# Kernel optimization log

Measured on AMD Instinct MI355X. Metric: run time of the kernel, lower is better.

## Reference

```python
import jax, jax.numpy as jnp
import numpy as np
import math

D_MODEL = 512
NUM_HEADS = 8
D_K = D_MODEL // NUM_HEADS
B, S = 8, 2048


def setup_inputs() -> dict:
    key = jax.random.key(0)
    ks = jax.random.split(key, 13)
    inv = 1.0 / math.sqrt(D_MODEL)
    def lin(kw, kb):
        W = jax.random.uniform(kw, (D_MODEL, D_MODEL), jnp.float32, -inv, inv)
        b = jax.random.uniform(kb, (D_MODEL,), jnp.float32, -inv, inv)
        return W, b
    Wq, bq = lin(ks[0], ks[1])
    Wk, bk = lin(ks[2], ks[3])
    Wv, bv = lin(ks[4], ks[5])
    Wo, bo = lin(ks[6], ks[7])
    Q = jax.random.normal(ks[8], (B, S, D_MODEL), jnp.float32)
    K = jax.random.normal(ks[9], (B, S, D_MODEL), jnp.float32)
    V = jax.random.normal(ks[10], (B, S, D_MODEL), jnp.float32)
    mask = jax.random.randint(ks[11], (1, 1, S, S), 0, 2, jnp.int32)
    return {"Q": Q, "K": K, "V": V, "mask": mask,
            "Wq": Wq, "bq": bq, "Wk": Wk, "bk": bk,
            "Wv": Wv, "bv": bv, "Wo": Wo, "bo": bo}


def _split_heads(x):
    b, s, _ = x.shape
    return x.reshape(b, s, NUM_HEADS, D_K).transpose(0, 2, 1, 3)  # [B,H,S,dk]


def reference(Q, K, V, mask, Wq, bq, Wk, bk, Wv, bv, Wo, bo):
    # Linear projections (torch Linear: x @ W^T + b) then head split
    q = _split_heads(Q @ Wq.T + bq)
    k = _split_heads(K @ Wk.T + bk)
    v = _split_heads(V @ Wv.T + bv)
    scores = jnp.einsum("bhqd,bhkd->bhqk", q, k) / math.sqrt(D_K)
    # masked_fill(mask == 0, -1e30) for float32
    scores = jnp.where(mask == 0, jnp.float32(-1e30), scores)
    probs = jax.nn.softmax(scores, axis=-1)
    # dropout in eval mode == identity
    out = jnp.einsum("bhqk,bhkd->bhqd", probs, v)
    out = out.transpose(0, 2, 1, 3).reshape(Q.shape[0], -1, D_MODEL)
    return out @ Wo.T + bo
```

## Files before the change

kernel.cpp:

```cpp
#include <hip/hip_runtime.h>
#include <hip/hip_bf16.h>
#include <math.h>

#define BB 8
#define SS 2048
#define HH 8
#define DKK 64
#define DM 512

typedef short bf16x8 __attribute__((ext_vector_type(8)));
typedef short bf16x4 __attribute__((ext_vector_type(4)));
typedef float f32x4 __attribute__((ext_vector_type(4)));
#define MFMA16(a, b, c) __builtin_amdgcn_mfma_f32_16x16x32_bf16(a, b, c, 0, 0, 0)

#if __has_builtin(__builtin_amdgcn_exp2f)
#define EXP2(x) __builtin_amdgcn_exp2f(x)
#else
#define EXP2(x) exp2f(x)
#endif

__device__ __forceinline__ unsigned short f2bf(float f) {
    __hip_bfloat16 h = __float2bfloat16(f);
    return *reinterpret_cast<unsigned short*>(&h);
}

__device__ __forceinline__ float max3f(float a, float b, float c) {
    return fmaxf(fmaxf(a, b), c);
}

__device__ __forceinline__ uint4 cvt8(const float* __restrict__ src) {
    float4 a = *(const float4*)src;
    float4 b = *(const float4*)(src + 4);
    unsigned short tmp[8];
    tmp[0] = f2bf(a.x); tmp[1] = f2bf(a.y); tmp[2] = f2bf(a.z); tmp[3] = f2bf(a.w);
    tmp[4] = f2bf(b.x); tmp[5] = f2bf(b.y); tmp[6] = f2bf(b.z); tmp[7] = f2bf(b.w);
    return *(uint4*)tmp;
}

__global__ __launch_bounds__(256) void mask_pack(
    const int* __restrict__ mask, unsigned long long* __restrict__ mb)
{
    const int t = threadIdx.x;
    const int wid = (blockIdx.x << 2) | (t >> 6);
    const int lane = t & 63;
    const int q = wid >> 5;
    const int c = wid & 31;
    int e = mask[(size_t)q * SS + (c << 6) + lane];
    unsigned long long bal = __ballot(e != 0);
    if (lane == 0) mb[wid] = bal;
}

__global__ __launch_bounds__(256) void w_cvt(
    const float* __restrict__ Wq, const float* __restrict__ Wk,
    const float* __restrict__ Wv, unsigned short* __restrict__ dst)
{
    const int idx = blockIdx.x * 256 + threadIdx.x;
    const int which = idx >> 15;
    const int off = (idx & 32767) * 8;
    const float* src = (which == 0) ? Wq : (which == 1) ? Wk : Wv;
    *(uint4*)(dst + (size_t)which * 262144 + off) = cvt8(src + off);
}

__global__ __launch_bounds__(256, 2) void proj_qkv_fused(
    const float* __restrict__ Xq, const float* __restrict__ Xk, const float* __restrict__ Xv,
    const unsigned short* __restrict__ Wb,
    const float* __restrict__ bq, const float* __restrict__ bk, const float* __restrict__ bv,
    unsigned short* __restrict__ outbase, float qscale)
{
    const int z = blockIdx.z;
    const float* X = (z == 0) ? Xq : (z == 1) ? Xk : Xv;
    const unsigned short* W = Wb + (size_t)z * 262144;
    const float* bias = (z == 0) ? bq : (z == 1) ? bk : bv;
    unsigned short* out = outbase + (size_t)z * ((size_t)BB * HH * SS * DKK);
    const float scale = (z == 0) ? qscale : 1.0f;

    __shared__ __align__(16) unsigned short Xs[128][72];
    __shared__ __align__(16) unsigned short Ws[128][72];
    const int t = threadIdx.x;
    const int w = t >> 6, l = t & 63;
    const int l15 = l & 15, lg = l >> 4;
    const int n0 = blockIdx.x * 128, m0 = blockIdx.y * 128;
    const int mo = (w & 1) * 64, no = (w >> 1) * 64;

    f32x4 acc[4][4];
#pragma unroll
    for (int i = 0; i < 4; i++)
#pragma unroll
        for (int j = 0; j < 4; j++) acc[i][j] = (f32x4){0.f, 0.f, 0.f, 0.f};

    for (int k0 = 0; k0 < DM; k0 += 64) {
        __syncthreads();
#pragma unroll
        for (int rr = 0; rr < 4; rr++) {
            int idx = rr * 2048 + t * 8;
            int row = idx >> 6, col = idx & 63;
            *(uint4*)&Xs[row][col] = cvt8(X + (size_t)(m0 + row) * DM + k0 + col);
            *(uint4*)&Ws[row][col] = *(const uint4*)(W + (size_t)(n0 + row) * DM + k0 + col);
        }
        __syncthreads();

        bf16x8 af[4][2], bfr[4][2];
#pragma unroll
        for (int mt = 0; mt < 4; mt++) {
            af[mt][0] = *(const bf16x8*)&Xs[mo + mt * 16 + l15][lg * 8];
            af[mt][1] = *(const bf16x8*)&Xs[mo + mt * 16 + l15][32 + lg * 8];
        }
#pragma unroll
        for (int nt = 0; nt < 4; nt++) {
            bfr[nt][0] = *(const bf16x8*)&Ws[no + nt * 16 + l15][lg * 8];
            bfr[nt][1] = *(const bf16x8*)&Ws[no + nt * 16 + l15][32 + lg * 8];
        }
#pragma unroll
        for (int mt = 0; mt < 4; mt++)
#pragma unroll
            for (int nt = 0; nt < 4; nt++) {
                acc[mt][nt] = MFMA16(af[mt][0], bfr[nt][0], acc[mt][nt]);
                acc[mt][nt] = MFMA16(af[mt][1], bfr[nt][1], acc[mt][nt]);
            }
    }

    float bv4[4];
#pragma unroll
    for (int nt = 0; nt < 4; nt++) bv4[nt] = bias[n0 + no + nt * 16 + l15];

    const int h = (n0 + no) >> 6;
    if (z == 2) {
#pragma unroll
        for (int mt = 0; mt < 4; mt++) {
            int m = m0 + mo + mt * 16 + lg * 4;
            int bb = m >> 11, s = m & (SS - 1);
#pragma unroll
            for (int nt = 0; nt < 4; nt++) {
                int d = nt * 16 + l15;
                bf16x4 pk;
#pragma unroll
                for (int r = 0; r < 4; r++) pk[r] = (short)f2bf(acc[mt][nt][r] + bv4[nt]);
                *(bf16x4*)(out + (((size_t)bb * HH + h) * DKK + d) * SS + s) = pk;
            }
        }
    } else {
#pragma unroll
        for (int mt = 0; mt < 4; mt++)
#pragma unroll
            for (int nt = 0; nt < 4; nt++)
#pragma unroll
                for (int r = 0; r < 4; r++) {
                    int m = m0 + mo + mt * 16 + lg * 4 + r;
                    int d = nt * 16 + l15;
                    float v = (acc[mt][nt][r] + bv4[nt]) * scale;
                    int bb = m >> 11, s = m & (SS - 1);
                    out[(((size_t)bb * HH + h) * SS + s) * 64 + d] = f2bf(v);
                }
    }
}

__global__ __launch_bounds__(256, 2) void proj_out_mfma(
    const unsigned short* __restrict__ Xb,
    const float* __restrict__ W,
    const float* __restrict__ bias,
    float* __restrict__ out)
{
    __shared__ __align__(16) unsigned short Xs[128][72];
    __shared__ __align__(16) unsigned short Ws[128][72];
    const int t = threadIdx.x;
    const int w = t >> 6, l = t & 63;
    const int l15 = l & 15, lg = l >> 4;
    const int n0 = blockIdx.x * 128, m0 = blockIdx.y * 128;
    const int mo = (w & 1) * 64, no = (w >> 1) * 64;

    f32x4 acc[4][4];
#pragma unroll
    for (int i = 0; i < 4; i++)
#pragma unroll
        for (int j = 0; j < 4; j++) acc[i][j] = (f32x4){0.f, 0.f, 0.f, 0.f};

    for (int k0 = 0; k0 < DM; k0 += 64) {
        __syncthreads();
#pragma unroll
        for (int rr = 0; rr < 4; rr++) {
            int idx = rr * 2048 + t * 8;
            int row = idx >> 6, col = idx & 63;
            *(uint4*)&Xs[row][col] = *(const uint4*)(Xb + (size_t)(m0 + row) * DM + k0 + col);
            *(uint4*)&Ws[row][col] = cvt8(W + (size_t)(n0 + row) * DM + k0 + col);
        }
        __syncthreads();

        bf16x8 af[4][2], bfr[4][2];
#pragma unroll
        for (int mt = 0; mt < 4; mt++) {
            af[mt][0] = *(const bf16x8*)&Xs[mo + mt * 16 + l15][lg * 8];
            af[mt][1] = *(const bf16x8*)&Xs[mo + mt * 16 + l15][32 + lg * 8];
        }
#pragma unroll
        for (int nt = 0; nt < 4; nt++) {
            bfr[nt][0] = *(const bf16x8*)&Ws[no + nt * 16 + l15][lg * 8];
            bfr[nt][1] = *(const bf16x8*)&Ws[no + nt * 16 + l15][32 + lg * 8];
        }
#pragma unroll
        for (int mt = 0; mt < 4; mt++)
#pragma unroll
            for (int nt = 0; nt < 4; nt++) {
                acc[mt][nt] = MFMA16(af[mt][0], bfr[nt][0], acc[mt][nt]);
                acc[mt][nt] = MFMA16(af[mt][1], bfr[nt][1], acc[mt][nt]);
            }
    }

    float bv4[4];
#pragma unroll
    for (int nt = 0; nt < 4; nt++) bv4[nt] = bias[n0 + no + nt * 16 + l15];

#pragma unroll
    for (int mt = 0; mt < 4; mt++)
#pragma unroll
        for (int nt = 0; nt < 4; nt++)
#pragma unroll
            for (int r = 0; r < 4; r++) {
                int m = m0 + mo + mt * 16 + lg * 4 + r;
                int n = n0 + no + nt * 16 + l15;
                out[(size_t)m * DM + n] = acc[mt][nt][r] + bv4[nt];
            }
}

__global__ __launch_bounds__(512, 4) void attn_kernel(
    const unsigned short* __restrict__ qw, const unsigned short* __restrict__ kw,
    const unsigned short* __restrict__ vtw,
    const unsigned long long* __restrict__ mb,
    unsigned short* __restrict__ ao)
{
    __shared__ __align__(16) unsigned short Ks[64][72];
    __shared__ __align__(16) unsigned short Vt[64][72];
    __shared__ __align__(16) unsigned short Pw[8 * 32 * 64];
    const int t = threadIdx.x;
    const int w = t >> 6, l = t & 63;
    const int l15 = l & 15, lg = l >> 4;
    const int q0 = blockIdx.x * 256;
    const int bh = blockIdx.y;
    const int b = bh >> 3, h = bh & 7;
    const int q0w = q0 + w * 32;
    const unsigned short* qb = qw + (size_t)bh * SS * DKK;
    const unsigned short* kb = kw + (size_t)bh * SS * DKK;
    const unsigned short* vtb = vtw + (size_t)bh * DKK * SS;

    const unsigned long long* mbq[2];
#pragma unroll
    for (int qt = 0; qt < 2; qt++)
        mbq[qt] = mb + ((size_t)(q0w + qt * 16 + l15) << 5);

    bf16x8 Qf[2][2];
#pragma unroll
    for (int qt = 0; qt < 2; qt++)
#pragma unroll
        for (int dh = 0; dh < 2; dh++)
            Qf[qt][dh] = *(const bf16x8*)(qb + (size_t)(q0w + qt * 16 + l15) * DKK + dh * 32 + lg * 8);

    f32x4 O[2][4];
    f32x4 Osum[2];
#pragma unroll
    for (int i = 0; i < 2; i++) {
#pragma unroll
        for (int j = 0; j < 4; j++) O[i][j] = (f32x4){0.f, 0.f, 0.f, 0.f};
        Osum[i] = (f32x4){0.f, 0.f, 0.f, 0.f};
    }
    float m_i[2];
#pragma unroll
    for (int i = 0; i < 2; i++) m_i[i] = -INFINITY;

    const bf16x8 vone = {16256, 16256, 16256, 16256, 16256, 16256, 16256, 16256};
    const int pbase = w * 2048;

    for (int kv0 = 0; kv0 < SS; kv0 += 64) {
        __syncthreads();
        {
            int idx = t * 8;
            int row = idx >> 6, col = idx & 63;
            *(uint4*)&Ks[row][col] = *(const uint4*)(kb + (size_t)(kv0 + row) * DKK + col);
            *(uint4*)&Vt[row][col] = *(const uint4*)(vtb + (size_t)row * SS + kv0 + col);
        }
        __syncthreads();

        f32x4 S[4][2];
#pragma unroll
        for (int kvt = 0; kvt < 4; kvt++) {
            bf16x8 ak0 = *(const bf16x8*)&Ks[kvt * 16 + l15][lg * 8];
            bf16x8 ak1 = *(const bf16x8*)&Ks[kvt * 16 + l15][32 + lg * 8];
#pragma unroll
            for (int qt = 0; qt < 2; qt++) {
                f32x4 z = (f32x4){0.f, 0.f, 0.f, 0.f};
                z = MFMA16(ak0, Qf[qt][0], z);
                z = MFMA16(ak1, Qf[qt][1], z);
                S[kvt][qt] = z;
            }
        }

#pragma unroll
        for (int qt = 0; qt < 2; qt++) {
            unsigned long long mm = mbq[qt][kv0 >> 6];
            unsigned int wlo = (unsigned int)mm;
            unsigned int whi = (unsigned int)(mm >> 32);
            unsigned int u[4];
            u[0] = wlo >> (lg * 4);
            u[1] = wlo >> (16 + lg * 4);
            u[2] = whi >> (lg * 4);
            u[3] = whi >> (16 + lg * 4);
#pragma unroll
            for (int kvt = 0; kvt < 4; kvt++) {
                if (!(u[kvt] & 1u)) S[kvt][qt][0] = -1e38f;
                if (!(u[kvt] & 2u)) S[kvt][qt][1] = -1e38f;
                if (!(u[kvt] & 4u)) S[kvt][qt][2] = -1e38f;
                if (!(u[kvt] & 8u)) S[kvt][qt][3] = -1e38f;
            }
        }

        float mtl[2];
#pragma unroll
        for (int qt = 0; qt < 2; qt++) {
            float mt = fmaxf(
                max3f(max3f(S[0][qt][0], S[0][qt][1], S[0][qt][2]),
                      max3f(S[0][qt][3], S[1][qt][0], S[1][qt][1]),
                      max3f(S[1][qt][2], S[1][qt][3], S[2][qt][0])),
                fmaxf(max3f(S[2][qt][1], S[2][qt][2], S[2][qt][3]),
                      max3f(S[3][qt][0], S[3][qt][1], fmaxf(S[3][qt][2], S[3][qt][3]))));
            mt = fmaxf(mt, __shfl_xor(mt, 16));
            mt = fmaxf(mt, __shfl_xor(mt, 32));
            mtl[qt] = mt;
        }
        int grow = (mtl[0] > m_i[0]) | (mtl[1] > m_i[1]);
        if (__any(grow)) {
            float alpha[2];
#pragma unroll
            for (int qt = 0; qt < 2; qt++) {
                float mn = fmaxf(m_i[qt], mtl[qt]);
                alpha[qt] = EXP2(m_i[qt] - mn);
                m_i[qt] = mn;
            }
#pragma unroll
            for (int qt = 0; qt < 2; qt++)
#pragma unroll
                for (int r = 0; r < 4; r++) {
                    float a = __shfl(alpha[qt], lg * 4 + r);
#pragma unroll
                    for (int dt = 0; dt < 4; dt++) O[qt][dt][r] *= a;
                    Osum[qt][r] *= a;
                }
        }

#pragma unroll
        for (int qt = 0; qt < 2; qt++) {
            const int prow = qt * 16 + l15;
            const int swz = (prow & 7) << 3;
#pragma unroll
            for (int kvt = 0; kvt < 4; kvt++) {
                float p0 = EXP2(S[kvt][qt][0] - m_i[qt]);
                float p1 = EXP2(S[kvt][qt][1] - m_i[qt]);
                float p2 = EXP2(S[kvt][qt][2] - m_i[qt]);
                float p3 = EXP2(S[kvt][qt][3] - m_i[qt]);
                bf16x4 pk;
                pk[0] = (short)f2bf(p0); pk[1] = (short)f2bf(p1);
                pk[2] = (short)f2bf(p2); pk[3] = (short)f2bf(p3);
                *(bf16x4*)&Pw[pbase + prow * 64 + ((kvt * 16 + lg * 4) ^ swz)] = pk;
            }
        }

        asm volatile("s_waitcnt lgkmcnt(0)" ::: "memory");

        bf16x8 bv2[4][2];
#pragma unroll
        for (int dt = 0; dt < 4; dt++) {
            bv2[dt][0] = *(const bf16x8*)&Vt[dt * 16 + l15][lg * 8];
            bv2[dt][1] = *(const bf16x8*)&Vt[dt * 16 + l15][32 + lg * 8];
        }
#pragma unroll
        for (int qt = 0; qt < 2; qt++) {
            const int prow = qt * 16 + l15;
            const int swz = (prow & 7) << 3;
            bf16x8 ap0 = *(const bf16x8*)&Pw[pbase + prow * 64 + ((lg * 8) ^ swz)];
            bf16x8 ap1 = *(const bf16x8*)&Pw[pbase + prow * 64 + ((32 + lg * 8) ^ swz)];
#pragma unroll
            for (int dt = 0; dt < 4; dt++) {
                O[qt][dt] = MFMA16(ap0, bv2[dt][0], O[qt][dt]);
                O[qt][dt] = MFMA16(ap1, bv2[dt][1], O[qt][dt]);
            }
            Osum[qt] = MFMA16(ap0, vone, Osum[qt]);
            Osum[qt] = MFMA16(ap1, vone, Osum[qt]);
        }
    }

#pragma unroll
    for (int qt = 0; qt < 2; qt++) {
#pragma unroll
        for (int r = 0; r < 4; r++) {
            float lv = 1.f / Osum[qt][r];
            int q = q0w + qt * 16 + lg * 4 + r;
            size_t base = ((size_t)b * SS + q) * DM + h * 64;
#pragma unroll
            for (int dt = 0; dt < 4; dt++)
                ao[base + dt * 16 + l15] = f2bf(O[qt][dt][r] * lv);
        }
    }
}

extern "C" void kernel_launch(void* const* d_in, const int* in_sizes, int n_in,
                              void* d_out, int out_size, void* d_ws, size_t ws_size,
                              hipStream_t stream) {
    const float* Q    = (const float*)d_in[0];
    const float* K    = (const float*)d_in[1];
    const float* V    = (const float*)d_in[2];
    const int*   mask = (const int*)d_in[3];
    const float* Wq   = (const float*)d_in[4];
    const float* bq   = (const float*)d_in[5];
    const float* Wk   = (const float*)d_in[6];
    const float* bk   = (const float*)d_in[7];
    const float* Wv   = (const float*)d_in[8];
    const float* bv   = (const float*)d_in[9];
    const float* Wo   = (const float*)d_in[10];
    const float* bo   = (const float*)d_in[11];

    const size_t SEG = (size_t)BB * HH * SS * DKK;
    unsigned short* qb  = (unsigned short*)d_ws;
    unsigned short* kb  = qb + SEG;
    unsigned short* vtb = kb + SEG;
    unsigned short* ab  = vtb + SEG;
    unsigned short* wb  = ab;

    const size_t MB_BYTES = (size_t)SS * (SS / 64) * sizeof(unsigned long long);
    unsigned long long* mbits =
        (unsigned long long*)((char*)d_out + (size_t)out_size - MB_BYTES);

    const float qscale = 0.125f * 1.44269504088896340736f;

    mask_pack<<<dim3((SS * (SS / 64)) / 4), 256, 0, stream>>>(mask, mbits);
    w_cvt<<<dim3(384), 256, 0, stream>>>(Wq, Wk, Wv, wb);

    dim3 gp(DM / 128, (BB * SS) / 128, 3);
    proj_qkv_fused<<<gp, 256, 0, stream>>>(Q, K, V, wb, bq, bk, bv, qb, qscale);

    attn_kernel<<<dim3(SS / 256, BB * HH), 512, 0, stream>>>(qb, kb, vtb, mbits, ab);

    proj_out_mfma<<<dim3(DM / 128, (BB * SS) / 128), 256, 0, stream>>>(ab, Wo, bo, (float*)d_out);
}
```

Baseline: 375.5 us.

## Double-buffer K/V tiles via direct global-to-LDS loads with XOR swizzle

```diff
diff --git a/kernel.cpp b/kernel.cpp
--- a/kernel.cpp
+++ b/kernel.cpp
@@ -18,6 +18,11 @@
 #else
 #define EXP2(x) exp2f(x)
 #endif
+
+#define GLL16(gsrc, ldst)                                                      \
+    __builtin_amdgcn_global_load_lds(                                          \
+        (const __attribute__((address_space(1))) unsigned int*)(gsrc),         \
+        (__attribute__((address_space(3))) unsigned int*)(ldst), 16, 0, 0)
 
 __device__ __forceinline__ unsigned short f2bf(float f) {
     __hip_bfloat16 h = __float2bfloat16(f);
@@ -227,8 +232,8 @@
     const unsigned long long* __restrict__ mb,
     unsigned short* __restrict__ ao)
 {
-    __shared__ __align__(16) unsigned short Ks[64][72];
-    __shared__ __align__(16) unsigned short Vt[64][72];
+    __shared__ __align__(16) unsigned short Kb[2][64 * 64];
+    __shared__ __align__(16) unsigned short Vb[2][64 * 64];
     __shared__ __align__(16) unsigned short Pw[8 * 32 * 64];
     const int t = threadIdx.x;
     const int w = t >> 6, l = t & 63;
@@ -241,6 +246,14 @@
     const unsigned short* kb = kw + (size_t)bh * SS * DKK;
     const unsigned short* vtb = vtw + (size_t)bh * DKK * SS;
 
+    const int srow = (w << 3) | (l >> 3);
+    const int schunk = (l & 7) ^ (srow & 7);
+    const size_t koff = (size_t)srow * DKK + schunk * 8;
+    const size_t voff = (size_t)srow * SS + schunk * 8;
+    const int ldsbase = w * 512;
+    const int co0 = ((lg ^ (l15 & 7)) * 8);
+    const int co1 = (((4 + lg) ^ (l15 & 7)) * 8);
+
     const unsigned long long* mbq[2];
 #pragma unroll
     for (int qt = 0; qt < 2; qt++)
@@ -268,21 +281,24 @@
     const bf16x8 vone = {16256, 16256, 16256, 16256, 16256, 16256, 16256, 16256};
     const int pbase = w * 2048;
 
+    GLL16(kb + koff, &Kb[0][ldsbase]);
+    GLL16(vtb + voff, &Vb[0][ldsbase]);
+    __syncthreads();
+
+    int cur = 0;
     for (int kv0 = 0; kv0 < SS; kv0 += 64) {
-        __syncthreads();
-        {
-            int idx = t * 8;
-            int row = idx >> 6, col = idx & 63;
-            *(uint4*)&Ks[row][col] = *(const uint4*)(kb + (size_t)(kv0 + row) * DKK + col);
-            *(uint4*)&Vt[row][col] = *(const uint4*)(vtb + (size_t)row * SS + kv0 + col);
-        }
-        __syncthreads();
-
+        if (kv0 + 64 < SS) {
+            GLL16(kb + (size_t)(kv0 + 64) * DKK + koff, &Kb[cur ^ 1][ldsbase]);
+            GLL16(vtb + (kv0 + 64) + voff, &Vb[cur ^ 1][ldsbase]);
+        }
+
+        const unsigned short* Kc = &Kb[cur][0];
+        const unsigned short* Vc = &Vb[cur][0];
         f32x4 S[4][2];
 #pragma unroll
         for (int kvt = 0; kvt < 4; kvt++) {
-            bf16x8 ak0 = *(const bf16x8*)&Ks[kvt * 16 + l15][lg * 8];
-            bf16x8 ak1 = *(const bf16x8*)&Ks[kvt * 16 + l15][32 + lg * 8];
+            bf16x8 ak0 = *(const bf16x8*)&Kc[(kvt * 16 + l15) * 64 + co0];
+            bf16x8 ak1 = *(const bf16x8*)&Kc[(kvt * 16 + l15) * 64 + co1];
 #pragma unroll
             for (int qt = 0; qt < 2; qt++) {
                 f32x4 z = (f32x4){0.f, 0.f, 0.f, 0.f};
@@ -366,8 +382,8 @@
         bf16x8 bv2[4][2];
 #pragma unroll
         for (int dt = 0; dt < 4; dt++) {
-            bv2[dt][0] = *(const bf16x8*)&Vt[dt * 16 + l15][lg * 8];
-            bv2[dt][1] = *(const bf16x8*)&Vt[dt * 16 + l15][32 + lg * 8];
+            bv2[dt][0] = *(const bf16x8*)&Vc[(dt * 16 + l15) * 64 + co0];
+            bv2[dt][1] = *(const bf16x8*)&Vc[(dt * 16 + l15) * 64 + co1];
         }
 #pragma unroll
         for (int qt = 0; qt < 2; qt++) {
@@ -383,6 +399,9 @@
             Osum[qt] = MFMA16(ap0, vone, Osum[qt]);
             Osum[qt] = MFMA16(ap1, vone, Osum[qt]);
         }
+
+        __syncthreads();
+        cur ^= 1;
     }
 
 #pragma unroll
```

Result: slower. 387.4 us (+3.2%).

## Pre-convert Q and V inputs to bf16 in a merged prep kernel

Applied to the files above, without the earlier changes.

```diff
diff --git a/kernel.cpp b/kernel.cpp
--- a/kernel.cpp
+++ b/kernel.cpp
@@ -37,42 +37,54 @@
     return *(uint4*)tmp;
 }
 
-__global__ __launch_bounds__(256) void mask_pack(
-    const int* __restrict__ mask, unsigned long long* __restrict__ mb)
+__global__ __launch_bounds__(256) void prep_kernel(
+    const int* __restrict__ mask, unsigned long long* __restrict__ mb,
+    const float* __restrict__ Wq, const float* __restrict__ Wk,
+    const float* __restrict__ Wv, unsigned short* __restrict__ wdst,
+    const float* __restrict__ Xq, const float* __restrict__ Xv,
+    unsigned short* __restrict__ xqd, unsigned short* __restrict__ xvd)
 {
+    const int bid = blockIdx.x;
     const int t = threadIdx.x;
-    const int wid = (blockIdx.x << 2) | (t >> 6);
-    const int lane = t & 63;
-    const int q = wid >> 5;
-    const int c = wid & 31;
-    int e = mask[(size_t)q * SS + (c << 6) + lane];
-    unsigned long long bal = __ballot(e != 0);
-    if (lane == 0) mb[wid] = bal;
-}
-
-__global__ __launch_bounds__(256) void w_cvt(
-    const float* __restrict__ Wq, const float* __restrict__ Wk,
-    const float* __restrict__ Wv, unsigned short* __restrict__ dst)
+    if (bid < 16384) {
+        const int wid = (bid << 2) | (t >> 6);
+        const int lane = t & 63;
+        const int q = wid >> 5;
+        const int c = wid & 31;
+        int e = mask[(size_t)q * SS + (c << 6) + lane];
+        unsigned long long bal = __ballot(e != 0);
+        if (lane == 0) mb[wid] = bal;
+    } else if (bid < 16768) {
+        const int idx = (bid - 16384) * 256 + t;
+        const int which = idx >> 15;
+        const int off = (idx & 32767) * 8;
+        const float* src = (which == 0) ? Wq : (which == 1) ? Wk : Wv;
+        *(uint4*)(wdst + (size_t)which * 262144 + off) = cvt8(src + off);
+    } else if (bid < 20864) {
+        const size_t off = ((size_t)(bid - 16768) * 256 + t) * 8;
+        *(uint4*)(xqd + off) = cvt8(Xq + off);
+    } else {
+        const size_t off = ((size_t)(bid - 20864) * 256 + t) * 8;
+        *(uint4*)(xvd + off) = cvt8(Xv + off);
+    }
+}
+
+__global__ __launch_bounds__(256, 2) void proj_qkv(
+    const unsigned short* __restrict__ XqB, const float* __restrict__ XkF,
+    const unsigned short* __restrict__ XvB,
+    const unsigned short* __restrict__ Wb,
+    const float* __restrict__ bq, const float* __restrict__ bk,
+    const float* __restrict__ bv,
+    unsigned short* __restrict__ qout, unsigned short* __restrict__ kout,
+    unsigned short* __restrict__ vtout,
+    float qscale, int mode0)
 {
-    const int idx = blockIdx.x * 256 + threadIdx.x;
-    const int which = idx >> 15;
-    const int off = (idx & 32767) * 8;
-    const float* src = (which == 0) ? Wq : (which == 1) ? Wk : Wv;
-    *(uint4*)(dst + (size_t)which * 262144 + off) = cvt8(src + off);
-}
-
-__global__ __launch_bounds__(256, 2) void proj_qkv_fused(
-    const float* __restrict__ Xq, const float* __restrict__ Xk, const float* __restrict__ Xv,
-    const unsigned short* __restrict__ Wb,
-    const float* __restrict__ bq, const float* __restrict__ bk, const float* __restrict__ bv,
-    unsigned short* __restrict__ outbase, float qscale)
-{
-    const int z = blockIdx.z;
-    const float* X = (z == 0) ? Xq : (z == 1) ? Xk : Xv;
-    const unsigned short* W = Wb + (size_t)z * 262144;
-    const float* bias = (z == 0) ? bq : (z == 1) ? bk : bv;
-    unsigned short* out = outbase + (size_t)z * ((size_t)BB * HH * SS * DKK);
-    const float scale = (z == 0) ? qscale : 1.0f;
+    const int mode = mode0 + blockIdx.z;
+    const unsigned short* XB = (mode == 0) ? XqB : XvB;
+    const float* bias = (mode == 0) ? bq : (mode == 1) ? bk : bv;
+    unsigned short* out = (mode == 0) ? qout : (mode == 1) ? kout : vtout;
+    const unsigned short* W = Wb + (size_t)mode * 262144;
+    const float scale = (mode == 0) ? qscale : 1.0f;
 
     __shared__ __align__(16) unsigned short Xs[128][72];
     __shared__ __align__(16) unsigned short Ws[128][72];
@@ -94,7 +106,10 @@
         for (int rr = 0; rr < 4; rr++) {
             int idx = rr * 2048 + t * 8;
             int row = idx >> 6, col = idx & 63;
-            *(uint4*)&Xs[row][col] = cvt8(X + (size_t)(m0 + row) * DM + k0 + col);
+            if (mode == 1)
+                *(uint4*)&Xs[row][col] = cvt8(XkF + (size_t)(m0 + row) * DM + k0 + col);
+            else
+                *(uint4*)&Xs[row][col] = *(const uint4*)(XB + (size_t)(m0 + row) * DM + k0 + col);
             *(uint4*)&Ws[row][col] = *(const uint4*)(W + (size_t)(n0 + row) * DM + k0 + col);
         }
         __syncthreads();
@@ -124,7 +139,7 @@
     for (int nt = 0; nt < 4; nt++) bv4[nt] = bias[n0 + no + nt * 16 + l15];
 
     const int h = (n0 + no) >> 6;
-    if (z == 2) {
+    if (mode == 2) {
 #pragma unroll
         for (int mt = 0; mt < 4; mt++) {
             int m = m0 + mo + mt * 16 + lg * 4;
@@ -420,19 +435,21 @@
     unsigned short* kb  = qb + SEG;
     unsigned short* vtb = kb + SEG;
     unsigned short* ab  = vtb + SEG;
-    unsigned short* wb  = ab;
-
+
+    unsigned short* wb = (unsigned short*)d_out;
     const size_t MB_BYTES = (size_t)SS * (SS / 64) * sizeof(unsigned long long);
     unsigned long long* mbits =
         (unsigned long long*)((char*)d_out + (size_t)out_size - MB_BYTES);
 
     const float qscale = 0.125f * 1.44269504088896340736f;
 
-    mask_pack<<<dim3((SS * (SS / 64)) / 4), 256, 0, stream>>>(mask, mbits);
-    w_cvt<<<dim3(384), 256, 0, stream>>>(Wq, Wk, Wv, wb);
-
-    dim3 gp(DM / 128, (BB * SS) / 128, 3);
-    proj_qkv_fused<<<gp, 256, 0, stream>>>(Q, K, V, wb, bq, bk, bv, qb, qscale);
+    prep_kernel<<<dim3(24960), 256, 0, stream>>>(mask, mbits, Wq, Wk, Wv, wb,
+                                                 Q, V, vtb, ab);
+
+    proj_qkv<<<dim3(DM / 128, (BB * SS) / 128, 1), 256, 0, stream>>>(
+        vtb, K, ab, wb, bq, bk, bv, qb, kb, vtb, qscale, 0);
+    proj_qkv<<<dim3(DM / 128, (BB * SS) / 128, 2), 256, 0, stream>>>(
+        vtb, K, ab, wb, bq, bk, bv, qb, kb, vtb, qscale, 1);
 
     attn_kernel<<<dim3(SS / 256, BB * HH), 512, 0, stream>>>(qb, kb, vtb, mbits, ab);
 
```

New measurement: 408.4 us. +8.8%, slower.
